# Kernel optimization log

Measured on AMD Instinct MI355X. Metric: run time of the kernel, lower is better.

## Reference

```python
import jax, jax.numpy as jnp
import numpy as np

DIM_IN, DIM_OUT, DIM_INNER = 1024, 1024, 128
SCALE = DIM_INNER ** -0.5


def setup_inputs() -> dict:
    key = jax.random.key(0)
    k1, k2, k3, k4 = jax.random.split(key, 4)
    x = jax.random.normal(k1, (4, 4096, DIM_IN), dtype=jnp.float32)
    # torch nn.Linear stores weight as [out, in]; we keep that layout and transpose in matmul
    w_qkv = jax.random.normal(k2, (3 * DIM_INNER, DIM_IN), dtype=jnp.float32) * (DIM_IN ** -0.5)
    w_out = jax.random.normal(k3, (DIM_OUT, DIM_INNER), dtype=jnp.float32) * (DIM_INNER ** -0.5)
    b_out = jax.random.normal(k4, (DIM_OUT,), dtype=jnp.float32) * 0.02
    return {"x": x, "w_qkv": w_qkv, "w_out": w_out, "b_out": b_out}


def reference(x, w_qkv, w_out, b_out):
    # qkv projection (no bias)
    qkv = jnp.einsum('bnd,ed->bne', x, w_qkv)            # [b, n, 3*dim_inner]
    q, k, v = jnp.split(qkv, 3, axis=-1)                 # each [b, n, dim_inner]
    sim = jnp.einsum('bid,bjd->bij', q, k) * SCALE       # [b, n, n]
    n = sim.shape[-1]
    causal = jnp.triu(jnp.ones((n, n), dtype=bool), 1)   # True above diagonal
    neg = jnp.finfo(q.dtype).max
    sim = jnp.where(causal[None, :, :], -neg, sim)
    attn = jax.nn.softmax(sim, axis=-1)
    out = jnp.einsum('bij,bjd->bid', attn, v)            # [b, n, dim_inner]
    return jnp.einsum('bnd,od->bno', out, w_out) + b_out # [b, n, dim_out]
```

## Files before the change

### kernel.cpp

```cpp
#include <hip/hip_runtime.h>
#include <math.h>


typedef __attribute__((ext_vector_type(8))) short bf16x8;
typedef __attribute__((ext_vector_type(4))) short bf16x4;
typedef __attribute__((ext_vector_type(4))) float f32x4;

#define FA_SCL2 0.12751886525137387f

__device__ __forceinline__ unsigned short f2bf(float f) {
    __bf16 h = (__bf16)f;
    return __builtin_bit_cast(unsigned short, h);
}
__device__ __forceinline__ float bf2f(unsigned short h) {
    union { unsigned u; float f; } v; v.u = ((unsigned)h) << 16;
    return v.f;
}
__device__ __forceinline__ f32x4 mfma16(bf16x8 a, bf16x8 b, f32x4 c) {
    return __builtin_amdgcn_mfma_f32_16x16x32_bf16(a, b, c, 0, 0, 0);
}
__device__ __forceinline__ void gl2lds16(const void* g, void* l) {
    __builtin_amdgcn_global_load_lds(
        (const __attribute__((address_space(1))) unsigned int*)g,
        (__attribute__((address_space(3))) unsigned int*)l, 16, 0, 0);
}
__device__ __forceinline__ f32x4 vmax4(f32x4 a, f32x4 b) {
    return f32x4{fmaxf(a[0], b[0]), fmaxf(a[1], b[1]),
                 fmaxf(a[2], b[2]), fmaxf(a[3], b[3])};
}

__global__ __launch_bounds__(256)
void wcast_all(const float* __restrict__ Wq, const float* __restrict__ Wo,
               unsigned short* __restrict__ wfm, unsigned short* __restrict__ wofm)
{
    const int bx = blockIdx.x, tid = threadIdx.x;
    if (bx < 192) {
        const int idx = bx * 256 + tid;
        const int kc = idx & 127, r = idx >> 7;
        const float* g = Wq + (size_t)r * 1024 + kc * 8;
        float4 w0 = *(const float4*)g, w1 = *(const float4*)(g + 4);
        bf16x8 p;
        p[0] = (short)f2bf(w0.x); p[1] = (short)f2bf(w0.y);
        p[2] = (short)f2bf(w0.z); p[3] = (short)f2bf(w0.w);
        p[4] = (short)f2bf(w1.x); p[5] = (short)f2bf(w1.y);
        p[6] = (short)f2bf(w1.z); p[7] = (short)f2bf(w1.w);
        *(bf16x8*)&wfm[(size_t)(kc * 384 + r) * 8] = p;
    } else {
        const int idx = (bx - 192) * 256 + tid;
        const int c = idx & 15, rg = idx >> 4;
        const float* g = Wo + (size_t)rg * 128 + c * 8;
        float4 w0 = *(const float4*)g, w1 = *(const float4*)(g + 4);
        bf16x8 p;
        p[0] = (short)f2bf(w0.x); p[1] = (short)f2bf(w0.y);
        p[2] = (short)f2bf(w0.z); p[3] = (short)f2bf(w0.w);
        p[4] = (short)f2bf(w1.x); p[5] = (short)f2bf(w1.y);
        p[6] = (short)f2bf(w1.z); p[7] = (short)f2bf(w1.w);
        *(bf16x8*)&wofm[((size_t)((rg >> 6) * 16 + c) * 64 + (rg & 63)) * 8] = p;
    }
}

__global__ __launch_bounds__(256, 3)
void gemm_qkv(const float* __restrict__ X, const unsigned short* __restrict__ Wfm,
              unsigned short* __restrict__ qfm, unsigned short* __restrict__ kfm,
              unsigned short* __restrict__ vfm)
{
    __shared__ unsigned short Asl[4096];
    __shared__ unsigned short Bsl[2][8192];
    const int tid = threadIdx.x;
    const int wv = tid >> 6, lane = tid & 63;
    const int lm = lane & 15, quad = lane >> 4;
    const int mt = blockIdx.x & 255;
    const int nt = blockIdx.x >> 8;
    const int mb = mt * 64, nb = nt * 128;
    const int wr = wv >> 1, wc = wv & 1;

    const int arow = tid >> 3, af8 = tid & 7;
    const float* gxr = X + (size_t)(mb + arow) * 1024 + af8 * 8;
    const int sg0 = (af8 * 64 + (arow ^ af8)) * 8;
    const int sg1 = sg0 + 32 * 8;

    f32x4 acc[2][4];
    #pragma unroll
    for (int i = 0; i < 2; ++i)
        #pragma unroll
        for (int j = 0; j < 4; ++j) acc[i][j] = f32x4{0.f, 0.f, 0.f, 0.f};

    auto loadA = [&](int it, float4& r0, float4& r1, float4& r2, float4& r3) {
        const float* g = gxr + it * 64;
        r0 = *(const float4*)g;
        r1 = *(const float4*)(g + 4);
        r2 = *(const float4*)(g + 32 * 1024);
        r3 = *(const float4*)(g + 32 * 1024 + 4);
    };
    auto stageA = [&](const float4& r0, const float4& r1,
                      const float4& r2, const float4& r3) {
        bf16x8 p0, p1;
        p0[0] = (short)f2bf(r0.x); p0[1] = (short)f2bf(r0.y);
        p0[2] = (short)f2bf(r0.z); p0[3] = (short)f2bf(r0.w);
        p0[4] = (short)f2bf(r1.x); p0[5] = (short)f2bf(r1.y);
        p0[6] = (short)f2bf(r1.z); p0[7] = (short)f2bf(r1.w);
        *(bf16x8*)&Asl[sg0] = p0;
        p1[0] = (short)f2bf(r2.x); p1[1] = (short)f2bf(r2.y);
        p1[2] = (short)f2bf(r2.z); p1[3] = (short)f2bf(r2.w);
        p1[4] = (short)f2bf(r3.x); p1[5] = (short)f2bf(r3.y);
        p1[6] = (short)f2bf(r3.z); p1[7] = (short)f2bf(r3.w);
        *(bf16x8*)&Asl[sg1] = p1;
    };
    auto issueB = [&](int it, int buf) {
        #pragma unroll
        for (int i = 0; i < 4; ++i) {
            const int p = wv * 4 + i;
            const int kc = p >> 1, colh = (p & 1) * 64;
            gl2lds16(Wfm + ((size_t)(it * 8 + kc) * 384 + nb + colh + lane) * 8,
                     &Bsl[buf][(kc * 128 + colh) * 8]);
        }
    };

    float4 a0, a1, a2, a3, b0, b1, b2, b3;
    loadA(0, a0, a1, a2, a3);
    issueB(0, 0);
    loadA(1, b0, b1, b2, b3);

    auto step = [&](const int i, float4& r0, float4& r1, float4& r2, float4& r3) {
        __builtin_amdgcn_s_barrier();
        stageA(r0, r1, r2, r3);
        if (i < 15) issueB(i + 1, (i + 1) & 1);
        if (i < 14) {
            loadA(i + 2, r0, r1, r2, r3);
            asm volatile("s_waitcnt vmcnt(12) lgkmcnt(0)" ::: "memory");
        } else if (i == 14) {
            asm volatile("s_waitcnt vmcnt(8) lgkmcnt(0)" ::: "memory");
        } else {
            asm volatile("s_waitcnt vmcnt(0) lgkmcnt(0)" ::: "memory");
        }
        __builtin_amdgcn_s_barrier();
        const unsigned short* Bc = Bsl[i & 1];
        bf16x8 af[2][2], bfr[2][4];
        #pragma unroll
        for (int s = 0; s < 2; ++s) {
            const int kc = s * 4 + quad;
            #pragma unroll
            for (int ii = 0; ii < 2; ++ii)
                af[s][ii] = *(const bf16x8*)
                    &Asl[(kc * 64 + ((wr * 32 + ii * 16 + lm) ^ kc)) * 8];
            #pragma unroll
            for (int j = 0; j < 4; ++j)
                bfr[s][j] = *(const bf16x8*)&Bc[(kc * 128 + wc * 64 + j * 16 + lm) * 8];
        }
        #pragma unroll
        for (int s = 0; s < 2; ++s)
            #pragma unroll
            for (int ii = 0; ii < 2; ++ii)
                #pragma unroll
                for (int j = 0; j < 4; ++j)
                    acc[ii][j] = mfma16(af[s][ii], bfr[s][j], acc[ii][j]);
    };

    for (int p = 0; p < 8; ++p) {
        step(2 * p,     a0, a1, a2, a3);
        step(2 * p + 1, b0, b1, b2, b3);
    }

    if (nt == 2) {
        unsigned short* T = &Bsl[0][0];
        __syncthreads();
        #pragma unroll
        for (int ii = 0; ii < 2; ++ii)
            #pragma unroll
            for (int j = 0; j < 4; ++j) {
                const int d = wc * 64 + j * 16 + lm;
                const int k0 = wr * 32 + ii * 16 + quad * 4;
                bf16x4 v;
                v[0] = (short)f2bf(acc[ii][j][0]);
                v[1] = (short)f2bf(acc[ii][j][1]);
                v[2] = (short)f2bf(acc[ii][j][2]);
                v[3] = (short)f2bf(acc[ii][j][3]);
                *(bf16x4*)&T[d * 72 + k0] = v;
            }
        __syncthreads();
        unsigned short* dst = vfm + (size_t)mt * 8192;
        #pragma unroll
        for (int t = 0; t < 4; ++t) {
            const int g = tid + t * 256;
            const int d = g & 127, c = g >> 7;
            bf16x8 x = *(const bf16x8*)&T[d * 72 + c * 8];
            *(bf16x8*)(dst + (size_t)(c * 128 + d) * 8) = x;
        }
    } else {
        unsigned short* dst = nt ? kfm : qfm;
        const float scl = nt ? 1.f : FA_SCL2;
        #pragma unroll
        for (int ii = 0; ii < 2; ++ii)
            #pragma unroll
            for (int j = 0; j < 4; ++j) {
                const int ncol = wc * 64 + j * 16 + lm;
                const size_t cb = ((size_t)mt * 16 + (ncol >> 3)) * 512 + (ncol & 7);
                #pragma unroll
                for (int r = 0; r < 4; ++r)
                    dst[cb + (size_t)(wr * 32 + ii * 16 + quad * 4 + r) * 8]
                        = f2bf(acc[ii][j][r] * scl);
            }
    }
}

__global__ __launch_bounds__(512, 4)
void flash_attn3(const unsigned short* __restrict__ Qfm, const unsigned short* __restrict__ Kfm,
                 const unsigned short* __restrict__ Vfm,
                 unsigned short* __restrict__ Opart, float* __restrict__ Ml)
{
    __shared__ unsigned short Klds[2][8192];
    __shared__ unsigned short Vlds[2][8192];
    __shared__ unsigned short Plds[8][1024];

    const int tid = threadIdx.x;
    const int wv = tid >> 6, lane = tid & 63;
    const int lm = lane & 15, quad = lane >> 4;

    const int bx = blockIdx.x;
    const int xcd = bx & 7;
    const int b   = xcd >> 1;
    const int r   = (bx >> 3) * 2 + (xcd & 1);
    const int sp  = r & 3;
    const int Qi  = (r < 64) ? (16 + (r >> 2)) : (15 - ((r - 64) >> 2));
    const int n   = 2 * Qi + 2;
    const int cnt = (n >> 2) + ((sp < (n & 3)) ? 1 : 0);
    const int ktb = sp * (n >> 2) + ((sp < (n & 3)) ? sp : (n & 3));
    const int kte = ktb + cnt;
    const int qtw = 2 * Qi + (wv >> 2);
    const int rw  = (wv & 3) * 16;

    const int qt0 = 2 * Qi;
    const size_t ob0 = (size_t)((b * 64 + qt0) * 4 + sp) * 8192;
    const size_t ob1 = ob0 + 4 * 8192;
    const int mlb0 = ((b * 64 + qt0) * 4 + sp) * 128, mlb1 = mlb0 + 512;

    if (cnt == 0) {
        bf16x8 z = {0, 0, 0, 0, 0, 0, 0, 0};
        #pragma unroll
        for (int t = 0; t < 2; ++t) {
            *(bf16x8*)&Opart[ob0 + (size_t)(tid + t * 512) * 8] = z;
            *(bf16x8*)&Opart[ob1 + (size_t)(tid + t * 512) * 8] = z;
        }
        if (tid < 64) { Ml[mlb0 + tid] = -INFINITY; Ml[mlb1 + tid] = -INFINITY; }
        else if (tid < 128) { Ml[mlb0 + tid] = 0.f; Ml[mlb1 + tid] = 0.f; }
        return;
    }

    {
        const size_t qb = (size_t)(b * 64 + qt0) * 8192;
        #pragma unroll
        for (int i = 0; i < 4; ++i) {
            const int p = wv * 4 + i;
            gl2lds16(Qfm + qb + (size_t)p * 512 + lane * 8, &Klds[0][0] + p * 512);
        }
    }
    __syncthreads();
    bf16x8 qf[4];
    {
        const unsigned short* Qt = &Klds[wv >> 2][0];
        #pragma unroll
        for (int c = 0; c < 4; ++c)
            qf[c] = *(const bf16x8*)&Qt[((c * 4 + quad) * 64 + rw + lm) * 8];
    }
    asm volatile("s_waitcnt lgkmcnt(0)" ::: "memory");
    __builtin_amdgcn_s_barrier();

    {
        const size_t kb = (size_t)(b * 64 + ktb) * 8192;
        #pragma unroll
        for (int i = 0; i < 2; ++i) {
            const int pc = wv * 2 + i;
            gl2lds16(Kfm + kb + pc * 512 + lane * 8, &Klds[0][pc * 512]);
            gl2lds16(Vfm + kb + pc * 512 + lane * 8, &Vlds[0][pc * 512]);
        }
    }

    f32x4 oacc[8];
    #pragma unroll
    for (int oc = 0; oc < 8; ++oc) oacc[oc] = f32x4{0.f, 0.f, 0.f, 0.f};
    f32x4 m4 = f32x4{-INFINITY, -INFINITY, -INFINITY, -INFINITY};
    f32x4 lacc = f32x4{0.f, 0.f, 0.f, 0.f};
    unsigned short* Pw = Plds[wv];
    const short ONE = (short)0x3F80;
    const bf16x8 ONESB = {ONE, ONE, ONE, ONE, ONE, ONE, ONE, ONE};

    for (int kt = ktb; kt < kte; ++kt) {
        const int cu = (kt - ktb) & 1;
        __builtin_amdgcn_s_barrier();
        if (kt + 1 < kte) {
            const size_t kb = (size_t)(b * 64 + kt + 1) * 8192;
            #pragma unroll
            for (int i = 0; i < 2; ++i) {
                const int pc = wv * 2 + i;
                gl2lds16(Kfm + kb + pc * 512 + lane * 8, &Klds[cu ^ 1][pc * 512]);
                gl2lds16(Vfm + kb + pc * 512 + lane * 8, &Vlds[cu ^ 1][pc * 512]);
            }
            asm volatile("s_waitcnt vmcnt(4)" ::: "memory");
        } else {
            asm volatile("s_waitcnt vmcnt(0)" ::: "memory");
        }
        __builtin_amdgcn_s_barrier();
        if (kt > qtw) continue;

        const unsigned short* Kc = &Klds[cu][0];
        const unsigned short* Vc = &Vlds[cu][0];

        f32x4 sv[4];
        __builtin_amdgcn_s_setprio(1);
        #pragma unroll
        for (int ct = 0; ct < 4; ++ct) {
            f32x4 a = f32x4{0.f, 0.f, 0.f, 0.f};
            #pragma unroll
            for (int c = 0; c < 4; ++c) {
                bf16x8 kf = *(const bf16x8*)&Kc[((c * 4 + quad) * 64 + ct * 16 + lm) * 8];
                a = mfma16(qf[c], kf, a);
            }
            sv[ct] = a;
        }
        __builtin_amdgcn_s_setprio(0);
        if (kt == qtw) {
            #pragma unroll
            for (int ct = 0; ct < 4; ++ct) {
                const int dg = ct * 16 + lm - rw - quad * 4;
                #pragma unroll
                for (int rr = 0; rr < 4; ++rr)
                    if (dg > rr) sv[ct][rr] = -INFINITY;
            }
        }
        const f32x4 pmax = vmax4(vmax4(sv[0], sv[1]), vmax4(sv[2], sv[3]));
        const float dm = fmaxf(fmaxf(pmax[0] - m4[0], pmax[1] - m4[1]),
                               fmaxf(pmax[2] - m4[2], pmax[3] - m4[3]));
        if (!__all(dm <= 8.f)) {
            f32x4 rmax = pmax;
            #pragma unroll
            for (int d = 1; d < 16; d <<= 1) {
                f32x4 o;
                #pragma unroll
                for (int e = 0; e < 4; ++e) o[e] = __shfl_xor(rmax[e], d);
                rmax = vmax4(rmax, o);
            }
            const f32x4 mnew = vmax4(m4, rmax);
            f32x4 alpha;
            #pragma unroll
            for (int e = 0; e < 4; ++e) alpha[e] = __builtin_amdgcn_exp2f(m4[e] - mnew[e]);
            m4 = mnew;
            #pragma unroll
            for (int oc = 0; oc < 8; ++oc) oacc[oc] *= alpha;
            lacc *= alpha;
        }
        #pragma unroll
        for (int ct = 0; ct < 4; ++ct)
            #pragma unroll
            for (int rr = 0; rr < 4; ++rr)
                sv[ct][rr] = __builtin_amdgcn_exp2f(sv[ct][rr] - m4[rr]);
        #pragma unroll
        for (int ct = 0; ct < 4; ++ct) {
            const int cb = ((ct * 2 + (lm >> 3)) * 16 + quad * 4) * 8 + (lm & 7);
            #pragma unroll
            for (int rr = 0; rr < 4; ++rr)
                Pw[cb + rr * 8] = f2bf(sv[ct][rr]);
        }
        __builtin_amdgcn_s_setprio(1);
        #pragma unroll
        for (int s = 0; s < 2; ++s) {
            bf16x8 pf = *(const bf16x8*)&Pw[((s * 4 + quad) * 16 + lm) * 8];
            lacc = mfma16(pf, ONESB, lacc);
            #pragma unroll
            for (int oc = 0; oc < 8; ++oc) {
                bf16x8 vf = *(const bf16x8*)&Vc[((s * 4 + quad) * 128 + oc * 16 + lm) * 8];
                oacc[oc] = mfma16(pf, vf, oacc[oc]);
            }
        }
        __builtin_amdgcn_s_setprio(0);
    }

    const size_t obw = (size_t)((b * 64 + qtw) * 4 + sp) * 8192;
    const int mlw = ((b * 64 + qtw) * 4 + sp) * 128;
    #pragma unroll
    for (int oc = 0; oc < 8; ++oc) {
        const size_t cb = obw + (size_t)((oc * 2 + (lm >> 3)) * 64
                          + rw + quad * 4) * 8 + (lm & 7);
        #pragma unroll
        for (int rr = 0; rr < 4; ++rr)
            Opart[cb + rr * 8] = f2bf(oacc[oc][rr]);
    }
    if (lm == 0)
        #pragma unroll
        for (int rr = 0; rr < 4; ++rr) {
            const int row = rw + quad * 4 + rr;
            Ml[mlw + row] = m4[rr];
            Ml[mlw + 64 + row] = lacc[rr];
        }
}

__global__ __launch_bounds__(512, 2)
void gemm_outf(const unsigned short* __restrict__ Opart, const float* __restrict__ Ml,
               const unsigned short* __restrict__ Wofm, const float* __restrict__ bias,
               float* __restrict__ out)
{
    __shared__ unsigned short Asl[8192];
    __shared__ unsigned short Wl[2][16384];
    const int tid = threadIdx.x;
    const int wv = tid >> 6, lane = tid & 63;
    const int lm = lane & 15, quad = lane >> 4;
    const int aq = blockIdx.x;
    const int nt0 = blockIdx.y * 4;
    const size_t pbase = (size_t)aq * 4 * 8192;
    const int mlb = aq * 4 * 128;

    auto issueW = [&](int nt, int buf) {
        #pragma unroll
        for (int i = 0; i < 4; ++i) {
            const int p = wv * 4 + i;
            gl2lds16(Wofm + (size_t)((nt * 2 + (p >> 4)) * 16 + (p & 15)) * 512 + lane * 8,
                     &Wl[buf][p * 512]);
        }
    };
    issueW(nt0, 0);

    {
        const int r = tid & 63;
        float m[4], l[4];
        #pragma unroll
        for (int s = 0; s < 4; ++s) {
            m[s] = Ml[mlb + s * 128 + r];
            l[s] = Ml[mlb + s * 128 + 64 + r];
        }
        const float M = fmaxf(fmaxf(m[0], m[1]), fmaxf(m[2], m[3]));
        float a[4], den = 0.f;
        #pragma unroll
        for (int s = 0; s < 4; ++s) {
            a[s] = __builtin_amdgcn_exp2f(m[s] - M);
            den += a[s] * l[s];
        }
        const float rsc = 1.f / den;
        #pragma unroll
        for (int h = 0; h < 2; ++h) {
            const int g = tid + h * 512;
            float acc8[8] = {};
            #pragma unroll
            for (int s = 0; s < 4; ++s) {
                bf16x8 x = *(const bf16x8*)&Opart[pbase + (size_t)s * 8192 + (size_t)g * 8];
                #pragma unroll
                for (int e = 0; e < 8; ++e) acc8[e] += a[s] * bf2f((unsigned short)x[e]);
            }
            bf16x8 o;
            #pragma unroll
            for (int e = 0; e < 8; ++e) o[e] = f2bf(acc8[e] * rsc);
            *(bf16x8*)&Asl[g * 8] = o;
        }
    }
    __syncthreads();

    const int rw4 = (wv & 3) * 16;
    const int tl  = wv >> 2;
    bf16x8 af[4];
    #pragma unroll
    for (int kt = 0; kt < 4; ++kt)
        af[kt] = *(const bf16x8*)&Asl[((kt * 4 + quad) * 64 + rw4 + lm) * 8];

    for (int it = 0; it < 4; ++it) {
        const int nt = nt0 + it;
        const int buf = it & 1;
        if (it < 3) {
            asm volatile("s_waitcnt vmcnt(4)" ::: "memory");
        } else {
            asm volatile("s_waitcnt vmcnt(0)" ::: "memory");
        }
        __builtin_amdgcn_s_barrier();
        if (it < 3) issueW(nt + 1, buf ^ 1);

        f32x4 acc[4];
        #pragma unroll
        for (int j = 0; j < 4; ++j) acc[j] = f32x4{0.f, 0.f, 0.f, 0.f};
        #pragma unroll
        for (int kt = 0; kt < 4; ++kt)
            #pragma unroll
            for (int j = 0; j < 4; ++j) {
                bf16x8 bfr = *(const bf16x8*)
                    &Wl[buf][((tl * 16 + kt * 4 + quad) * 64 + j * 16 + lm) * 8];
                acc[j] = mfma16(af[kt], bfr, acc[j]);
            }
        #pragma unroll
        for (int j = 0; j < 4; ++j) {
            const int col = nt * 128 + tl * 64 + j * 16 + lm;
            const float bv = bias[col];
            #pragma unroll
            for (int rr = 0; rr < 4; ++rr) {
                const int m = aq * 64 + rw4 + quad * 4 + rr;
                out[(size_t)m * 1024 + col] = acc[j][rr] + bv;
            }
        }
        __builtin_amdgcn_s_barrier();
    }
}

extern "C" void kernel_launch(void* const* d_in, const int* in_sizes, int n_in,
                              void* d_out, int out_size, void* d_ws, size_t ws_size,
                              hipStream_t stream)
{
    (void)in_sizes; (void)n_in; (void)out_size; (void)ws_size;
    const float* x     = (const float*)d_in[0];
    const float* w_qkv = (const float*)d_in[1];
    const float* w_out = (const float*)d_in[2];
    const float* b_out = (const float*)d_in[3];
    float* out = (float*)d_out;
    unsigned short* ws = (unsigned short*)d_ws;

    const size_t NE = (size_t)16384 * 128;
    unsigned short* qfm = ws;
    unsigned short* kfm = ws + NE;
    unsigned short* wofm = ws + 2 * NE;
    unsigned short* vfm = ws + 3 * NE;
    unsigned short* op  = ws + 4 * NE;
    float*          ml  = (float*)(ws + 8 * NE);
    unsigned short* wfm = op;

    hipLaunchKernelGGL(wcast_all,   dim3(256),      dim3(256), 0, stream, w_qkv, w_out, wfm, wofm);
    hipLaunchKernelGGL(gemm_qkv,    dim3(768),      dim3(256), 0, stream, x, wfm, qfm, kfm, vfm);
    hipLaunchKernelGGL(flash_attn3, dim3(512),      dim3(512), 0, stream, qfm, kfm, vfm, op, ml);
    hipLaunchKernelGGL(gemm_outf,   dim3(256, 2),   dim3(512), 0, stream, op, ml, wofm, b_out, out);
}
```

Before: 175.0 us.

## Switch flash attention to 32x32x16 MFMA with 4 waves owning 32 rows each

Reworks the attention kernel so each of 4 waves (256 threads) handles 32 query rows using 32x32x16 bf16 MFMAs instead of 8 waves with 16-row 16x16x32 tiles. The P tile is stored to LDS with an XOR swizzle, and the softmax row reductions now span 32 lanes. The larger MFMA tiles are meant to raise operand reuse and cut LDS reads per flop. In exchange there are fewer waves per block, more accumulator registers, and a different LDS bank access pattern.

```diff
diff --git a/kernel.cpp b/kernel.cpp
--- a/kernel.cpp
+++ b/kernel.cpp
@@ -5,6 +5,7 @@
 typedef __attribute__((ext_vector_type(8))) short bf16x8;
 typedef __attribute__((ext_vector_type(4))) short bf16x4;
 typedef __attribute__((ext_vector_type(4))) float f32x4;
+typedef __attribute__((ext_vector_type(16))) float f32x16;
 
 #define FA_SCL2 0.12751886525137387f
 
@@ -18,15 +19,14 @@
 }
 __device__ __forceinline__ f32x4 mfma16(bf16x8 a, bf16x8 b, f32x4 c) {
     return __builtin_amdgcn_mfma_f32_16x16x32_bf16(a, b, c, 0, 0, 0);
+}
+__device__ __forceinline__ f32x16 mfma32(bf16x8 a, bf16x8 b, f32x16 c) {
+    return __builtin_amdgcn_mfma_f32_32x32x16_bf16(a, b, c, 0, 0, 0);
 }
 __device__ __forceinline__ void gl2lds16(const void* g, void* l) {
     __builtin_amdgcn_global_load_lds(
         (const __attribute__((address_space(1))) unsigned int*)g,
         (__attribute__((address_space(3))) unsigned int*)l, 16, 0, 0);
-}
-__device__ __forceinline__ f32x4 vmax4(f32x4 a, f32x4 b) {
-    return f32x4{fmaxf(a[0], b[0]), fmaxf(a[1], b[1]),
-                 fmaxf(a[2], b[2]), fmaxf(a[3], b[3])};
 }
 
 __global__ __launch_bounds__(256)
@@ -203,18 +203,18 @@
     }
 }
 
-__global__ __launch_bounds__(512, 4)
+__global__ __launch_bounds__(256)
 void flash_attn3(const unsigned short* __restrict__ Qfm, const unsigned short* __restrict__ Kfm,
                  const unsigned short* __restrict__ Vfm,
                  unsigned short* __restrict__ Opart, float* __restrict__ Ml)
 {
     __shared__ unsigned short Klds[2][8192];
     __shared__ unsigned short Vlds[2][8192];
-    __shared__ unsigned short Plds[8][1024];
+    __shared__ unsigned short Plds[4][2048];
 
     const int tid = threadIdx.x;
     const int wv = tid >> 6, lane = tid & 63;
-    const int lm = lane & 15, quad = lane >> 4;
+    const int l31 = lane & 31, lh = lane >> 5;
 
     const int bx = blockIdx.x;
     const int xcd = bx & 7;
@@ -226,10 +226,10 @@
     const int cnt = (n >> 2) + ((sp < (n & 3)) ? 1 : 0);
     const int ktb = sp * (n >> 2) + ((sp < (n & 3)) ? sp : (n & 3));
     const int kte = ktb + cnt;
-    const int qtw = 2 * Qi + (wv >> 2);
-    const int rw  = (wv & 3) * 16;
-
     const int qt0 = 2 * Qi;
+    const int qtw = qt0 + (wv >> 1);
+    const int rh  = (wv & 1) * 32;
+
     const size_t ob0 = (size_t)((b * 64 + qt0) * 4 + sp) * 8192;
     const size_t ob1 = ob0 + 4 * 8192;
     const int mlb0 = ((b * 64 + qt0) * 4 + sp) * 128, mlb1 = mlb0 + 512;
@@ -237,9 +237,9 @@
     if (cnt == 0) {
         bf16x8 z = {0, 0, 0, 0, 0, 0, 0, 0};
         #pragma unroll
-        for (int t = 0; t < 2; ++t) {
-            *(bf16x8*)&Opart[ob0 + (size_t)(tid + t * 512) * 8] = z;
-            *(bf16x8*)&Opart[ob1 + (size_t)(tid + t * 512) * 8] = z;
+        for (int t = 0; t < 4; ++t) {
+            *(bf16x8*)&Opart[ob0 + (size_t)(tid + t * 256) * 8] = z;
+            *(bf16x8*)&Opart[ob1 + (size_t)(tid + t * 256) * 8] = z;
         }
         if (tid < 64) { Ml[mlb0 + tid] = -INFINITY; Ml[mlb1 + tid] = -INFINITY; }
         else if (tid < 128) { Ml[mlb0 + tid] = 0.f; Ml[mlb1 + tid] = 0.f; }
@@ -249,18 +249,18 @@
     {
         const size_t qb = (size_t)(b * 64 + qt0) * 8192;
         #pragma unroll
-        for (int i = 0; i < 4; ++i) {
-            const int p = wv * 4 + i;
+        for (int i = 0; i < 8; ++i) {
+            const int p = wv * 8 + i;
             gl2lds16(Qfm + qb + (size_t)p * 512 + lane * 8, &Klds[0][0] + p * 512);
         }
     }
     __syncthreads();
-    bf16x8 qf[4];
+    bf16x8 qf[8];
     {
-        const unsigned short* Qt = &Klds[wv >> 2][0];
-        #pragma unroll
-        for (int c = 0; c < 4; ++c)
-            qf[c] = *(const bf16x8*)&Qt[((c * 4 + quad) * 64 + rw + lm) * 8];
+        const unsigned short* Qt = &Klds[0][0] + (wv >> 1) * 8192;
+        #pragma unroll
+        for (int m = 0; m < 8; ++m)
+            qf[m] = *(const bf16x8*)&Qt[((m * 2 + lh) * 64 + rh + l31) * 8];
     }
     asm volatile("s_waitcnt lgkmcnt(0)" ::: "memory");
     __builtin_amdgcn_s_barrier();
@@ -268,21 +268,25 @@
     {
         const size_t kb = (size_t)(b * 64 + ktb) * 8192;
         #pragma unroll
-        for (int i = 0; i < 2; ++i) {
-            const int pc = wv * 2 + i;
+        for (int i = 0; i < 4; ++i) {
+            const int pc = wv * 4 + i;
             gl2lds16(Kfm + kb + pc * 512 + lane * 8, &Klds[0][pc * 512]);
             gl2lds16(Vfm + kb + pc * 512 + lane * 8, &Vlds[0][pc * 512]);
         }
     }
 
-    f32x4 oacc[8];
+    f32x16 oacc[4];
     #pragma unroll
-    for (int oc = 0; oc < 8; ++oc) oacc[oc] = f32x4{0.f, 0.f, 0.f, 0.f};
-    f32x4 m4 = f32x4{-INFINITY, -INFINITY, -INFINITY, -INFINITY};
-    f32x4 lacc = f32x4{0.f, 0.f, 0.f, 0.f};
+    for (int dc = 0; dc < 4; ++dc)
+        #pragma unroll
+        for (int e = 0; e < 16; ++e) oacc[dc][e] = 0.f;
+    f32x16 m16, lacc;
+    #pragma unroll
+    for (int e = 0; e < 16; ++e) { m16[e] = -INFINITY; lacc[e] = 0.f; }
     unsigned short* Pw = Plds[wv];
     const short ONE = (short)0x3F80;
     const bf16x8 ONESB = {ONE, ONE, ONE, ONE, ONE, ONE, ONE, ONE};
+    const int swzr = (l31 & 7) << 3;
 
     for (int kt = ktb; kt < kte; ++kt) {
         const int cu = (kt - ktb) & 1;
@@ -290,12 +294,12 @@
         if (kt + 1 < kte) {
             const size_t kb = (size_t)(b * 64 + kt + 1) * 8192;
             #pragma unroll
-            for (int i = 0; i < 2; ++i) {
-                const int pc = wv * 2 + i;
+            for (int i = 0; i < 4; ++i) {
+                const int pc = wv * 4 + i;
                 gl2lds16(Kfm + kb + pc * 512 + lane * 8, &Klds[cu ^ 1][pc * 512]);
                 gl2lds16(Vfm + kb + pc * 512 + lane * 8, &Vlds[cu ^ 1][pc * 512]);
             }
-            asm volatile("s_waitcnt vmcnt(4)" ::: "memory");
+            asm volatile("s_waitcnt vmcnt(8)" ::: "memory");
         } else {
             asm volatile("s_waitcnt vmcnt(0)" ::: "memory");
         }
@@ -305,70 +309,73 @@
         const unsigned short* Kc = &Klds[cu][0];
         const unsigned short* Vc = &Vlds[cu][0];
 
-        f32x4 sv[4];
+        f32x16 s0, s1;
+        #pragma unroll
+        for (int e = 0; e < 16; ++e) { s0[e] = 0.f; s1[e] = 0.f; }
         __builtin_amdgcn_s_setprio(1);
         #pragma unroll
-        for (int ct = 0; ct < 4; ++ct) {
-            f32x4 a = f32x4{0.f, 0.f, 0.f, 0.f};
-            #pragma unroll
-            for (int c = 0; c < 4; ++c) {
-                bf16x8 kf = *(const bf16x8*)&Kc[((c * 4 + quad) * 64 + ct * 16 + lm) * 8];
-                a = mfma16(qf[c], kf, a);
-            }
-            sv[ct] = a;
+        for (int m = 0; m < 8; ++m) {
+            bf16x8 kf0 = *(const bf16x8*)&Kc[((m * 2 + lh) * 64 + l31) * 8];
+            bf16x8 kf1 = *(const bf16x8*)&Kc[((m * 2 + lh) * 64 + 32 + l31) * 8];
+            s0 = mfma32(qf[m], kf0, s0);
+            s1 = mfma32(qf[m], kf1, s1);
         }
         __builtin_amdgcn_s_setprio(0);
         if (kt == qtw) {
             #pragma unroll
-            for (int ct = 0; ct < 4; ++ct) {
-                const int dg = ct * 16 + lm - rw - quad * 4;
+            for (int reg = 0; reg < 16; ++reg) {
+                const int rowt = rh + (reg & 3) + 8 * (reg >> 2) + 4 * lh;
+                if (l31 > rowt)      s0[reg] = -INFINITY;
+                if (32 + l31 > rowt) s1[reg] = -INFINITY;
+            }
+        }
+        float dm = -INFINITY;
+        f32x16 pmax;
+        #pragma unroll
+        for (int e = 0; e < 16; ++e) {
+            pmax[e] = fmaxf(s0[e], s1[e]);
+            dm = fmaxf(dm, pmax[e] - m16[e]);
+        }
+        if (!__all(dm <= 8.f)) {
+            f32x16 rmax = pmax;
+            #pragma unroll
+            for (int d = 1; d < 32; d <<= 1)
                 #pragma unroll
-                for (int rr = 0; rr < 4; ++rr)
-                    if (dg > rr) sv[ct][rr] = -INFINITY;
-            }
-        }
-        const f32x4 pmax = vmax4(vmax4(sv[0], sv[1]), vmax4(sv[2], sv[3]));
-        const float dm = fmaxf(fmaxf(pmax[0] - m4[0], pmax[1] - m4[1]),
-                               fmaxf(pmax[2] - m4[2], pmax[3] - m4[3]));
-        if (!__all(dm <= 8.f)) {
-            f32x4 rmax = pmax;
-            #pragma unroll
-            for (int d = 1; d < 16; d <<= 1) {
-                f32x4 o;
-                #pragma unroll
-                for (int e = 0; e < 4; ++e) o[e] = __shfl_xor(rmax[e], d);
-                rmax = vmax4(rmax, o);
-            }
-            const f32x4 mnew = vmax4(m4, rmax);
-            f32x4 alpha;
-            #pragma unroll
-            for (int e = 0; e < 4; ++e) alpha[e] = __builtin_amdgcn_exp2f(m4[e] - mnew[e]);
-            m4 = mnew;
-            #pragma unroll
-            for (int oc = 0; oc < 8; ++oc) oacc[oc] *= alpha;
+                for (int e = 0; e < 16; ++e)
+                    rmax[e] = fmaxf(rmax[e], __shfl_xor(rmax[e], d));
+            f32x16 alpha;
+            #pragma unroll
+            for (int e = 0; e < 16; ++e) {
+                const float mn = fmaxf(m16[e], rmax[e]);
+                alpha[e] = __builtin_amdgcn_exp2f(m16[e] - mn);
+                m16[e] = mn;
+            }
+            #pragma unroll
+            for (int dc = 0; dc < 4; ++dc) oacc[dc] *= alpha;
             lacc *= alpha;
         }
         #pragma unroll
-        for (int ct = 0; ct < 4; ++ct)
-            #pragma unroll
-            for (int rr = 0; rr < 4; ++rr)
-                sv[ct][rr] = __builtin_amdgcn_exp2f(sv[ct][rr] - m4[rr]);
-        #pragma unroll
-        for (int ct = 0; ct < 4; ++ct) {
-            const int cb = ((ct * 2 + (lm >> 3)) * 16 + quad * 4) * 8 + (lm & 7);
-            #pragma unroll
-            for (int rr = 0; rr < 4; ++rr)
-                Pw[cb + rr * 8] = f2bf(sv[ct][rr]);
+        for (int e = 0; e < 16; ++e) {
+            s0[e] = __builtin_amdgcn_exp2f(s0[e] - m16[e]);
+            s1[e] = __builtin_amdgcn_exp2f(s1[e] - m16[e]);
+        }
+        #pragma unroll
+        for (int reg = 0; reg < 16; ++reg) {
+            const int R = (reg & 3) + 8 * (reg >> 2) + 4 * lh;
+            const int sw = (R & 7) << 3;
+            Pw[R * 64 + (l31 ^ sw)]        = f2bf(s0[reg]);
+            Pw[R * 64 + ((32 + l31) ^ sw)] = f2bf(s1[reg]);
         }
         __builtin_amdgcn_s_setprio(1);
         #pragma unroll
-        for (int s = 0; s < 2; ++s) {
-            bf16x8 pf = *(const bf16x8*)&Pw[((s * 4 + quad) * 16 + lm) * 8];
-            lacc = mfma16(pf, ONESB, lacc);
-            #pragma unroll
-            for (int oc = 0; oc < 8; ++oc) {
-                bf16x8 vf = *(const bf16x8*)&Vc[((s * 4 + quad) * 128 + oc * 16 + lm) * 8];
-                oacc[oc] = mfma16(pf, vf, oacc[oc]);
+        for (int s4 = 0; s4 < 4; ++s4) {
+            const int k0 = s4 * 16 + lh * 8;
+            bf16x8 pf = *(const bf16x8*)&Pw[l31 * 64 + (k0 ^ swzr)];
+            lacc = mfma32(pf, ONESB, lacc);
+            #pragma unroll
+            for (int dc = 0; dc < 4; ++dc) {
+                bf16x8 vf = *(const bf16x8*)&Vc[((s4 * 2 + lh) * 128 + dc * 32 + l31) * 8];
+                oacc[dc] = mfma32(pf, vf, oacc[dc]);
             }
         }
         __builtin_amdgcn_s_setprio(0);
@@ -377,19 +384,21 @@
     const size_t obw = (size_t)((b * 64 + qtw) * 4 + sp) * 8192;
     const int mlw = ((b * 64 + qtw) * 4 + sp) * 128;
     #pragma unroll
-    for (int oc = 0; oc < 8; ++oc) {
-        const size_t cb = obw + (size_t)((oc * 2 + (lm >> 3)) * 64
-                          + rw + quad * 4) * 8 + (lm & 7);
-        #pragma unroll
-        for (int rr = 0; rr < 4; ++rr)
-            Opart[cb + rr * 8] = f2bf(oacc[oc][rr]);
-    }
-    if (lm == 0)
-        #pragma unroll
-        for (int rr = 0; rr < 4; ++rr) {
-            const int row = rw + quad * 4 + rr;
-            Ml[mlw + row] = m4[rr];
-            Ml[mlw + 64 + row] = lacc[rr];
+    for (int dc = 0; dc < 4; ++dc) {
+        const int d = dc * 32 + l31;
+        const size_t cb = obw + (size_t)(d >> 3) * 512 + (d & 7);
+        #pragma unroll
+        for (int reg = 0; reg < 16; ++reg) {
+            const int row64 = rh + (reg & 3) + 8 * (reg >> 2) + 4 * lh;
+            Opart[cb + (size_t)row64 * 8] = f2bf(oacc[dc][reg]);
+        }
+    }
+    if (l31 == 0)
+        #pragma unroll
+        for (int reg = 0; reg < 16; ++reg) {
+            const int row64 = rh + (reg & 3) + 8 * (reg >> 2) + 4 * lh;
+            Ml[mlw + row64] = m16[reg];
+            Ml[mlw + 64 + row64] = lacc[reg];
         }
 }
 
@@ -518,6 +527,6 @@
 
     hipLaunchKernelGGL(wcast_all,   dim3(256),      dim3(256), 0, stream, w_qkv, w_out, wfm, wofm);
     hipLaunchKernelGGL(gemm_qkv,    dim3(768),      dim3(256), 0, stream, x, wfm, qfm, kfm, vfm);
-    hipLaunchKernelGGL(flash_attn3, dim3(512),      dim3(512), 0, stream, qfm, kfm, vfm, op, ml);
+    hipLaunchKernelGGL(flash_attn3, dim3(512),      dim3(256), 0, stream, qfm, kfm, vfm, op, ml);
     hipLaunchKernelGGL(gemm_outf,   dim3(256, 2),   dim3(512), 0, stream, op, ml, wofm, b_out, out);
 }
```

Result: slower. 191.9 us (+9.6%).
